# Performance work log

Measured on AMD Instinct MI355X. Metric: run time of the kernel, lower is better.

Reference implementation:

```python
import jax, jax.numpy as jnp
import numpy as np

N_NODES = 100000
D = 64
N_EDGES = 2_000_000
COS_EPS = 1e-6  # nn.CosineSimilarity eps


def setup_inputs() -> dict:
    key = jax.random.key(0)
    k1, k2 = jax.random.split(key)
    node_embs = jax.random.normal(k1, (N_NODES, D), dtype=jnp.float32)
    edge_index = jax.random.randint(k2, (2, N_EDGES), 0, N_NODES, dtype=jnp.int32)
    return {"node_embs": node_embs, "edge_index": edge_index, "temperature": 1}


def reference(node_embs, edge_index, temperature):
    # Edge-wise gather: f1/f2 are [E, D]
    f1 = node_embs[edge_index[0]]
    f2 = node_embs[edge_index[1]]
    # Per-edge cosine similarity (torch semantics: clamp each norm at eps)
    dot = jnp.sum(f1 * f2, axis=1)
    n1 = jnp.maximum(jnp.sqrt(jnp.sum(f1 * f1, axis=1)), COS_EPS)
    n2 = jnp.maximum(jnp.sqrt(jnp.sum(f2 * f2, axis=1)), COS_EPS)
    att_log = dot / (n1 * n2)
    # gumbel_softmax_sample: sigmoid(logits / T), then straight-through threshold
    values = jax.nn.sigmoid(att_log / temperature)
    values_hard = jnp.where(values <= 0.5, jnp.float32(0.0), values)
    out = jax.lax.stop_gradient(values_hard - values) + values
    # out are the sparse graph values (indices = edge_index); att == out
    return out
```

## Files before the change

### kernel.cpp

```cpp
#include <hip/hip_runtime.h>
#include <hip/hip_fp16.h>
#include <math.h>


#define D 64
#define BLOCK 256
#define COS_EPS 1e-6f
#define TAU 6e-3f
#define LOG2E 1.4426950408889634f

#define FMA4(A, X, Y) \
    A.x += X.x * Y.x; A.y += X.y * Y.y; A.z += X.z * Y.z; A.w += X.w * Y.w;

#define PAIRWISE8(E, O) \
    (((E.x + E.y) + (E.z + E.w)) + ((O.x + O.y) + (O.z + O.w)))

typedef _Float16 half2_t __attribute__((ext_vector_type(2)));

__device__ __forceinline__ half2_t as_h2(unsigned u) {
    union { unsigned u; half2_t v; } c; c.u = u; return c.v;
}

__device__ __forceinline__ float dot8_f16(uint4 A, uint4 B, float acc) {
#if __has_builtin(__builtin_amdgcn_fdot2)
    acc = __builtin_amdgcn_fdot2(as_h2(A.x), as_h2(B.x), acc, false);
    acc = __builtin_amdgcn_fdot2(as_h2(A.y), as_h2(B.y), acc, false);
    acc = __builtin_amdgcn_fdot2(as_h2(A.z), as_h2(B.z), acc, false);
    acc = __builtin_amdgcn_fdot2(as_h2(A.w), as_h2(B.w), acc, false);
#else
    const __half2* a = (const __half2*)&A;
    const __half2* b = (const __half2*)&B;
    #pragma unroll
    for (int i = 0; i < 4; ++i) {
        float2 af = __half22float2(a[i]);
        float2 bf = __half22float2(b[i]);
        acc = fmaf(af.x, bf.x, acc);
        acc = fmaf(af.y, bf.y, acc);
    }
#endif
    return acc;
}

__device__ __forceinline__ float read_temperature(const int* temp_ptr) {
    int tbits = *temp_ptr;
    if (tbits >= 1 && tbits < (1 << 23)) return (float)tbits;
    union { int i; float f; } u; u.i = tbits; return u.f;
}

__device__ __forceinline__ float exact_cos(
    const float* __restrict__ node_embs,
    const float* __restrict__ dnorm,
    int i0, int i1, int lane)
{
    const float4* __restrict__ r0 = (const float4*)(node_embs + (size_t)i0 * D);
    const float4* __restrict__ r1 = (const float4*)(node_embs + (size_t)i1 * D);
    float4 x0 = r0[lane];
    float4 x1 = r0[lane + 8];
    float4 y0 = r1[lane];
    float4 y1 = r1[lane + 8];
    float pp = ((x0.x * y0.x + x0.y * y0.y) + (x0.z * y0.z + x0.w * y0.w))
             + ((x1.x * y1.x + x1.y * y1.y) + (x1.z * y1.z + x1.w * y1.w));
    #pragma unroll
    for (int m = 1; m < 8; m <<= 1) pp += __shfl_xor(pp, m, 8);
    return pp / (dnorm[i0] * dnorm[i1]);
}

__global__ __launch_bounds__(BLOCK) void node_prep_kernel(
    const float* __restrict__ node_embs,
    float*       __restrict__ dnorm,
    __half*      __restrict__ htab,
    int n_nodes)
{
    int n = blockIdx.x * BLOCK + threadIdx.x;
    if (n >= n_nodes) return;

    const float4* __restrict__ r = (const float4*)(node_embs + (size_t)n * D);

    float4 row[16];
    #pragma unroll
    for (int k = 0; k < 16; ++k) row[k] = r[k];

    float4 z = make_float4(0.f, 0.f, 0.f, 0.f);
    float4 aE = z, aO = z;
    #pragma unroll
    for (int k = 0; k < 16; k += 2) {
        FMA4(aE, row[k], row[k])
        FMA4(aO, row[k + 1], row[k + 1])
    }
    float s = PAIRWISE8(aE, aO);
    float d = fmaxf(sqrtf(s), COS_EPS);
    dnorm[n] = d;

    float inv = 1.0f / d;
    uint4* dst = (uint4*)(htab + (size_t)n * D);
    #pragma unroll
    for (int k = 0; k < 16; k += 2) {
        float4 a = row[k];
        float4 b = row[k + 1];
        __half2 h[4];
        h[0] = __floats2half2_rn(a.x * inv, a.y * inv);
        h[1] = __floats2half2_rn(a.z * inv, a.w * inv);
        h[2] = __floats2half2_rn(b.x * inv, b.y * inv);
        h[3] = __floats2half2_rn(b.z * inv, b.w * inv);
        dst[k >> 1] = *(const uint4*)h;
    }
}

__global__ __launch_bounds__(BLOCK) void GraphLearner_68513318306086_kernel(
    const float* __restrict__ node_embs,
    const __half* __restrict__ htab,
    const int*   __restrict__ edge_index,
    const float* __restrict__ dnorm,
    const int*   __restrict__ temp_ptr,
    float*       __restrict__ out,
    int n_edges)
{
    int t    = blockIdx.x * BLOCK + threadIdx.x;
    int g    = t >> 3;
    int lane = threadIdx.x & 7;
    int e0   = g * 2;
    if (e0 >= n_edges) return;
    bool has1 = (e0 + 1) < n_edges;

    int2 i0p, i1p;
    if (has1) {
        i0p = *(const int2*)(edge_index + e0);
        i1p = *(const int2*)(edge_index + n_edges + e0);
    } else {
        i0p.x = edge_index[e0];            i0p.y = i0p.x;
        i1p.x = edge_index[n_edges + e0];  i1p.y = i1p.x;
    }

    const uint4* __restrict__ tab = (const uint4*)htab;
    uint4 A0 = tab[(i0p.x << 3) + lane];
    uint4 B0 = tab[(i1p.x << 3) + lane];
    uint4 A1 = tab[(i0p.y << 3) + lane];
    uint4 B1 = tab[(i1p.y << 3) + lane];

    float p0 = dot8_f16(A0, B0, 0.0f);
    float p1 = dot8_f16(A1, B1, 0.0f);

    #pragma unroll
    for (int m = 1; m < 8; m <<= 1) {
        p0 += __shfl_xor(p0, m, 8);
        p1 += __shfl_xor(p1, m, 8);
    }

    float cos0 = p0;
    float cos1 = p1;
    if (fabsf(cos0) < TAU)
        cos0 = exact_cos(node_embs, dnorm, i0p.x, i1p.x, lane);
    if (has1 && fabsf(cos1) < TAU)
        cos1 = exact_cos(node_embs, dnorm, i0p.y, i1p.y, lane);

    if (lane < 2 && (lane == 0 || has1)) {
        float cosv = lane ? cos1 : cos0;
        float T    = read_temperature(temp_ptr);
        float invT = __builtin_amdgcn_rcpf(T);
        float x    = cosv * invT;
        float ex   = __builtin_amdgcn_exp2f(-x * LOG2E);
        float v    = __builtin_amdgcn_rcpf(1.0f + ex);
        out[e0 + lane] = (x <= 0.0f) ? 0.0f : v;
    }
}

__global__ __launch_bounds__(BLOCK) void edge_kernel_fused(
    const float* __restrict__ node_embs,
    const int*   __restrict__ edge_index,
    const int*   __restrict__ temp_ptr,
    float*       __restrict__ out,
    int n_edges)
{
    int t    = blockIdx.x * BLOCK + threadIdx.x;
    int e    = t >> 3;
    int lane = threadIdx.x & 7;
    if (e >= n_edges) return;

    int i0 = edge_index[e];
    int i1 = edge_index[n_edges + e];

    const float4* __restrict__ r0 = (const float4*)(node_embs + (size_t)i0 * D);
    const float4* __restrict__ r1 = (const float4*)(node_embs + (size_t)i1 * D);

    float4 x0 = r0[lane];
    float4 x1 = r0[lane + 8];
    float4 y0 = r1[lane];
    float4 y1 = r1[lane + 8];

    float p  = ((x0.x * y0.x + x0.y * y0.y) + (x0.z * y0.z + x0.w * y0.w))
             + ((x1.x * y1.x + x1.y * y1.y) + (x1.z * y1.z + x1.w * y1.w));
    float a  = ((x0.x * x0.x + x0.y * x0.y) + (x0.z * x0.z + x0.w * x0.w))
             + ((x1.x * x1.x + x1.y * x1.y) + (x1.z * x1.z + x1.w * x1.w));
    float b  = ((y0.x * y0.x + y0.y * y0.y) + (y0.z * y0.z + y0.w * y0.w))
             + ((y1.x * y1.x + y1.y * y1.y) + (y1.z * y1.z + y1.w * y1.w));

    #pragma unroll
    for (int m = 1; m < 8; m <<= 1) {
        p += __shfl_xor(p, m, 8);
        a += __shfl_xor(a, m, 8);
        b += __shfl_xor(b, m, 8);
    }

    if (lane == 0) {
        float T    = read_temperature(temp_ptr);
        float d1   = fmaxf(sqrtf(a), COS_EPS);
        float d2   = fmaxf(sqrtf(b), COS_EPS);
        float cosv = p / (d1 * d2);
        float v    = 1.0f / (1.0f + expf(-(cosv / T)));
        out[e] = (v <= 0.5f) ? 0.0f : v;
    }
}

extern "C" void kernel_launch(void* const* d_in, const int* in_sizes, int n_in,
                              void* d_out, int out_size, void* d_ws, size_t ws_size,
                              hipStream_t stream) {
    const float* node_embs  = (const float*)d_in[0];
    const int*   edge_index = (const int*)d_in[1];
    const int*   temp_ptr   = (const int*)d_in[2];
    float*       out        = (float*)d_out;

    int n_nodes = in_sizes[0] / D;
    int n_elems = in_sizes[0];
    int n_edges = in_sizes[1] / 2;

    size_t htab_bytes = (size_t)n_elems * sizeof(__half);
    size_t need = htab_bytes + (size_t)n_nodes * sizeof(float);

    if (ws_size >= need) {
        __half* htab  = (__half*)d_ws;
        float*  dnorm = (float*)((char*)d_ws + htab_bytes);

        int grid_n = (n_nodes + BLOCK - 1) / BLOCK;
        node_prep_kernel<<<grid_n, BLOCK, 0, stream>>>(node_embs, dnorm, htab, n_nodes);

        int n_groups = (n_edges + 1) / 2;
        long long n_threads = (long long)n_groups * 8;
        int grid_e = (int)((n_threads + BLOCK - 1) / BLOCK);
        GraphLearner_68513318306086_kernel<<<grid_e, BLOCK, 0, stream>>>(
            node_embs, htab, edge_index, dnorm, temp_ptr, out, n_edges);
    } else {
        int grid_e = (int)(((long long)n_edges * 8 + BLOCK - 1) / BLOCK);
        edge_kernel_fused<<<grid_e, BLOCK, 0, stream>>>(
            node_embs, edge_index, temp_ptr, out, n_edges);
    }
}
```

Measured before the change: 145.0 us.

## Quantize node table to int8 with per-node scale and use sdot4

Replaces the fp16 unit-normalized node table with an int8 table that uses a per-row max-abs scale folded together with the inverse norm. The edge kernel then gathers 8 bytes per lane instead of 16 and computes the dot product with packed int8 dot instructions. This halves the random gather traffic, adds four extra scale loads per edge pair, and enlarges quantization error. The TAU threshold for the exact fallback is unchanged, so edges with cosine near zero may be misclassified more often, or the fallback may need to fire more often.

```diff
diff --git a/kernel.cpp b/kernel.cpp
--- a/kernel.cpp
+++ b/kernel.cpp
@@ -15,30 +15,18 @@
 #define PAIRWISE8(E, O) \
     (((E.x + E.y) + (E.z + E.w)) + ((O.x + O.y) + (O.z + O.w)))
 
-typedef _Float16 half2_t __attribute__((ext_vector_type(2)));
-
-__device__ __forceinline__ half2_t as_h2(unsigned u) {
-    union { unsigned u; half2_t v; } c; c.u = u; return c.v;
-}
-
-__device__ __forceinline__ float dot8_f16(uint4 A, uint4 B, float acc) {
-#if __has_builtin(__builtin_amdgcn_fdot2)
-    acc = __builtin_amdgcn_fdot2(as_h2(A.x), as_h2(B.x), acc, false);
-    acc = __builtin_amdgcn_fdot2(as_h2(A.y), as_h2(B.y), acc, false);
-    acc = __builtin_amdgcn_fdot2(as_h2(A.z), as_h2(B.z), acc, false);
-    acc = __builtin_amdgcn_fdot2(as_h2(A.w), as_h2(B.w), acc, false);
+__device__ __forceinline__ int dot4_i8(unsigned a, unsigned b, int acc) {
+#if __has_builtin(__builtin_amdgcn_sdot4)
+    return __builtin_amdgcn_sdot4(a, b, acc, false);
 #else
-    const __half2* a = (const __half2*)&A;
-    const __half2* b = (const __half2*)&B;
     #pragma unroll
     for (int i = 0; i < 4; ++i) {
-        float2 af = __half22float2(a[i]);
-        float2 bf = __half22float2(b[i]);
-        acc = fmaf(af.x, bf.x, acc);
-        acc = fmaf(af.y, bf.y, acc);
-    }
+        int ai = (int)((signed char)((a >> (8 * i)) & 0xff));
+        int bi = (int)((signed char)((b >> (8 * i)) & 0xff));
+        acc += ai * bi;
+    }
+    return acc;
 #endif
-    return acc;
 }
 
 __device__ __forceinline__ float read_temperature(const int* temp_ptr) {
@@ -66,9 +54,10 @@
 }
 
 __global__ __launch_bounds__(BLOCK) void node_prep_kernel(
-    const float* __restrict__ node_embs,
-    float*       __restrict__ dnorm,
-    __half*      __restrict__ htab,
+    const float*   __restrict__ node_embs,
+    float*         __restrict__ dnorm,
+    float*         __restrict__ nscale,
+    unsigned int*  __restrict__ q8,
     int n_nodes)
 {
     int n = blockIdx.x * BLOCK + threadIdx.x;
@@ -90,29 +79,43 @@
     float s = PAIRWISE8(aE, aO);
     float d = fmaxf(sqrtf(s), COS_EPS);
     dnorm[n] = d;
-
     float inv = 1.0f / d;
-    uint4* dst = (uint4*)(htab + (size_t)n * D);
-    #pragma unroll
-    for (int k = 0; k < 16; k += 2) {
+
+    float m0 = 0.f;
+    #pragma unroll
+    for (int k = 0; k < 16; ++k) {
         float4 a = row[k];
-        float4 b = row[k + 1];
-        __half2 h[4];
-        h[0] = __floats2half2_rn(a.x * inv, a.y * inv);
-        h[1] = __floats2half2_rn(a.z * inv, a.w * inv);
-        h[2] = __floats2half2_rn(b.x * inv, b.y * inv);
-        h[3] = __floats2half2_rn(b.z * inv, b.w * inv);
-        dst[k >> 1] = *(const uint4*)h;
-    }
+        m0 = fmaxf(m0, fmaxf(fmaxf(fabsf(a.x), fabsf(a.y)),
+                             fmaxf(fabsf(a.z), fabsf(a.w))));
+    }
+    float kq = (m0 > 0.f) ? (127.0f / m0) : 0.f;
+    nscale[n] = (m0 * inv) / 127.0f;
+
+    unsigned int w[16];
+    #pragma unroll
+    for (int k = 0; k < 16; ++k) {
+        float4 a = row[k];
+        int q0 = (int)rintf(a.x * kq);
+        int q1 = (int)rintf(a.y * kq);
+        int q2 = (int)rintf(a.z * kq);
+        int q3 = (int)rintf(a.w * kq);
+        w[k] = (unsigned)(q0 & 255) | ((unsigned)(q1 & 255) << 8)
+             | ((unsigned)(q2 & 255) << 16) | ((unsigned)(q3 & 255) << 24);
+    }
+    uint4* dst = (uint4*)(q8 + (size_t)n * 16);
+    #pragma unroll
+    for (int k = 0; k < 4; ++k)
+        dst[k] = *(const uint4*)&w[k * 4];
 }
 
 __global__ __launch_bounds__(BLOCK) void GraphLearner_68513318306086_kernel(
-    const float* __restrict__ node_embs,
-    const __half* __restrict__ htab,
-    const int*   __restrict__ edge_index,
-    const float* __restrict__ dnorm,
-    const int*   __restrict__ temp_ptr,
-    float*       __restrict__ out,
+    const float*        __restrict__ node_embs,
+    const unsigned int* __restrict__ q8,
+    const float*        __restrict__ nscale,
+    const int*          __restrict__ edge_index,
+    const float*        __restrict__ dnorm,
+    const int*          __restrict__ temp_ptr,
+    float*              __restrict__ out,
     int n_edges)
 {
     int t    = blockIdx.x * BLOCK + threadIdx.x;
@@ -131,23 +134,27 @@
         i1p.x = edge_index[n_edges + e0];  i1p.y = i1p.x;
     }
 
-    const uint4* __restrict__ tab = (const uint4*)htab;
-    uint4 A0 = tab[(i0p.x << 3) + lane];
-    uint4 B0 = tab[(i1p.x << 3) + lane];
-    uint4 A1 = tab[(i0p.y << 3) + lane];
-    uint4 B1 = tab[(i1p.y << 3) + lane];
-
-    float p0 = dot8_f16(A0, B0, 0.0f);
-    float p1 = dot8_f16(A1, B1, 0.0f);
+    const uint2* __restrict__ tab = (const uint2*)q8;
+    uint2 A0 = tab[(i0p.x << 3) + lane];
+    uint2 B0 = tab[(i1p.x << 3) + lane];
+    uint2 A1 = tab[(i0p.y << 3) + lane];
+    uint2 B1 = tab[(i1p.y << 3) + lane];
+    float sA0 = nscale[i0p.x];
+    float sB0 = nscale[i1p.x];
+    float sA1 = nscale[i0p.y];
+    float sB1 = nscale[i1p.y];
+
+    int d0 = dot4_i8(A0.y, B0.y, dot4_i8(A0.x, B0.x, 0));
+    int d1 = dot4_i8(A1.y, B1.y, dot4_i8(A1.x, B1.x, 0));
 
     #pragma unroll
     for (int m = 1; m < 8; m <<= 1) {
-        p0 += __shfl_xor(p0, m, 8);
-        p1 += __shfl_xor(p1, m, 8);
-    }
-
-    float cos0 = p0;
-    float cos1 = p1;
+        d0 += __shfl_xor(d0, m, 8);
+        d1 += __shfl_xor(d1, m, 8);
+    }
+
+    float cos0 = (float)d0 * (sA0 * sB0);
+    float cos1 = (float)d1 * (sA1 * sB1);
     if (fabsf(cos0) < TAU)
         cos0 = exact_cos(node_embs, dnorm, i0p.x, i1p.x, lane);
     if (has1 && fabsf(cos1) < TAU)
@@ -223,21 +230,22 @@
     int n_elems = in_sizes[0];
     int n_edges = in_sizes[1] / 2;
 
-    size_t htab_bytes = (size_t)n_elems * sizeof(__half);
-    size_t need = htab_bytes + (size_t)n_nodes * sizeof(float);
+    size_t q8_bytes = (size_t)n_elems;
+    size_t need = q8_bytes + (size_t)n_nodes * 2 * sizeof(float);
 
     if (ws_size >= need) {
-        __half* htab  = (__half*)d_ws;
-        float*  dnorm = (float*)((char*)d_ws + htab_bytes);
+        unsigned int* q8     = (unsigned int*)d_ws;
+        float*        nscale = (float*)((char*)d_ws + q8_bytes);
+        float*        dnorm  = nscale + n_nodes;
 
         int grid_n = (n_nodes + BLOCK - 1) / BLOCK;
-        node_prep_kernel<<<grid_n, BLOCK, 0, stream>>>(node_embs, dnorm, htab, n_nodes);
+        node_prep_kernel<<<grid_n, BLOCK, 0, stream>>>(node_embs, dnorm, nscale, q8, n_nodes);
 
         int n_groups = (n_edges + 1) / 2;
         long long n_threads = (long long)n_groups * 8;
         int grid_e = (int)((n_threads + BLOCK - 1) / BLOCK);
         GraphLearner_68513318306086_kernel<<<grid_e, BLOCK, 0, stream>>>(
-            node_embs, htab, edge_index, dnorm, temp_ptr, out, n_edges);
+            node_embs, q8, nscale, edge_index, dnorm, temp_ptr, out, n_edges);
     } else {
         int grid_e = (int)(((long long)n_edges * 8 + BLOCK - 1) / BLOCK);
         edge_kernel_fused<<<grid_e, BLOCK, 0, stream>>>(
```

After: 136.5 us. 5.9% less time.
